# Kernel optimization log

Hardware: AMD Instinct MI355X
Metric: run time of the kernel (lower is better)

## Reference

```python
import jax, jax.numpy as jnp
import numpy as np

EPS = 1e-5
BN_SCALE = 1.0 / np.sqrt(1.0 + EPS)  # inference BN with running_mean=0, running_var=1


def lrelu(x):
    return jnp.where(x >= 0, x, 0.2 * x)


def bn_affine(x, g, b, axis=1):
    shp = [1] * x.ndim
    shp[axis] = -1
    return x * (g.reshape(shp) * BN_SCALE) + b.reshape(shp)


def knn_idx(x, k):
    # x: (B, C, N) -> (B, N, k) indices of k nearest neighbors (incl. self)
    x2 = jnp.sum(x * x, axis=1)                       # (B, N)
    inner = jnp.einsum('bcn,bcm->bnm', x, x)          # (B, N, N)
    neg_dist = 2.0 * inner - x2[:, :, None] - x2[:, None, :]
    return jax.lax.top_k(neg_dist, k)[1]


def graph_feature(x, k):
    # x: (B, C, N) -> (B, 2C, N, k) edge features [x_j - x_i, x_i]
    B, C, N = x.shape
    idx = knn_idx(x, k)                               # (B, N, k)
    xt = jnp.transpose(x, (0, 2, 1))                  # (B, N, C)
    nbr = xt[jnp.arange(B)[:, None, None], idx]       # (B, N, k, C)
    ctr = xt[:, :, None, :]                           # (B, N, 1, C)
    feat = jnp.concatenate([nbr - ctr, jnp.broadcast_to(ctr, nbr.shape)], axis=-1)
    return jnp.transpose(feat, (0, 3, 1, 2))          # (B, 2C, N, k)


def edge_conv(x, W, g, b, k):
    # get_graph_feature -> 1x1 conv -> BN -> LeakyReLU -> max over neighbors
    f = graph_feature(x, k)
    h = jnp.einsum('oc,bcnk->bonk', W, f)
    return jnp.max(lrelu(bn_affine(h, g, b, axis=1)), axis=-1)  # (B, O, N)


def fps(xyz, m):
    # xyz: (B, 3, N) -> (B, m) farthest-point-sample indices, starting at index 0
    B, _, N = xyz.shape
    pts = jnp.transpose(xyz, (0, 2, 1))               # (B, N, 3)

    def body(carry, _):
        dists, last = carry
        p = jnp.take_along_axis(pts, last[:, None, None], axis=1)  # (B, 1, 3)
        d = jnp.sum((pts - p) ** 2, axis=-1)          # (B, N)
        dists = jnp.minimum(dists, d)
        nxt = jnp.argmax(dists, axis=-1).astype(jnp.int32)
        return (dists, nxt), last

    init = (jnp.full((B, N), 1e10, dtype=xyz.dtype), jnp.zeros((B,), jnp.int32))
    _, idxs = jax.lax.scan(body, init, None, length=m)
    return jnp.transpose(idxs, (1, 0))                # (B, m)


def gather_ch(x, idx):
    # x: (B, C, N), idx: (B, M) -> (B, C, M)
    B, C, _ = x.shape
    return jnp.take_along_axis(x, jnp.broadcast_to(idx[:, None, :], (B, C, idx.shape[1])), axis=2)


def aggregate(xyz, node, features, k):
    # xyz: (B,3,N), node: (B,3,M), features: (B,C,N) -> (B,C,M)
    B = xyz.shape[0]
    x2 = jnp.sum(xyz * xyz, axis=1)                   # (B, N)
    n2 = jnp.sum(node * node, axis=1)                 # (B, M)
    inner = jnp.einsum('bcm,bcn->bmn', node, xyz)     # (B, M, N)
    neg_d = 2.0 * inner - n2[:, :, None] - x2[:, None, :]
    idx = jax.lax.top_k(neg_d, k)[1]                  # (B, M, k) nearest points per node
    ft = jnp.transpose(features, (0, 2, 1))           # (B, N, C)
    grp = ft[jnp.arange(B)[:, None, None], idx]       # (B, M, k, C)
    return jnp.transpose(jnp.max(grp, axis=2), (0, 2, 1))  # (B, C, M)


def setup_inputs() -> dict:
    key = jax.random.key(0)
    ks = jax.random.split(key, 32)
    B, N, K, E = 8, 2048, 20, 1024

    def w(k_, o, c):
        return jax.random.normal(k_, (o, c), jnp.float32) / np.sqrt(c)

    def gb(k_, c):
        k1, k2 = jax.random.split(k_)
        return (jax.random.uniform(k1, (c,), jnp.float32, 0.5, 1.5),
                0.1 * jax.random.normal(k2, (c,), jnp.float32))

    g1, b1 = gb(ks[1], 64); g2, b2 = gb(ks[2], 64); g2m, b2m = gb(ks[3], E)
    g3, b3 = gb(ks[4], 256); g4, b4 = gb(ks[5], 256); g5, b5 = gb(ks[6], E)
    g6, b6 = gb(ks[7], 512); g7, b7 = gb(ks[8], 256)
    return {
        'x': jax.random.normal(ks[0], (B, 3, N), jnp.float32),
        'W1': w(ks[10], 64, 6), 'g1': g1, 'b1': b1,
        'W2': w(ks[11], 64, 128), 'g2': g2, 'b2': b2,
        'W2m': w(ks[12], E, 128), 'g2m': g2m, 'b2m': b2m,
        'W3': w(ks[13], 256, 512), 'g3': g3, 'b3': b3,
        'W4': w(ks[14], 256, 512), 'g4': g4, 'b4': b4,
        'W5': w(ks[15], E, 512), 'g5': g5, 'b5': b5,
        'Wl1': w(ks[16], 512, 2 * E), 'g6': g6, 'b6': b6,
        'Wl2': w(ks[17], 256, 512), 'bl2': 0.01 * jax.random.normal(ks[18], (256,), jnp.float32),
        'g7': g7, 'b7': b7,
        'Wl3': w(ks[19], 40, 256), 'bl3': 0.01 * jax.random.normal(ks[20], (40,), jnp.float32),
    }


def reference(x, W1, g1, b1, W2, g2, b2, W2m, g2m, b2m, W3, g3, b3,
              W4, g4, b4, W5, g5, b5, Wl1, g6, b6, Wl2, bl2, g7, b7, Wl3, bl3):
    K = 20
    B, _, N = x.shape
    xyz = x

    x1 = edge_conv(x, W1, g1, b1, K)                  # (B, 64, N)
    x2 = edge_conv(x1, W2, g2, b2, K)                 # (B, 64, N)
    xt1_ = jnp.concatenate([x1, x2], axis=1)          # (B, 128, N)
    xt1 = lrelu(bn_affine(jnp.einsum('oc,bcn->bon', W2m, xt1_), g2m, b2m, axis=1))

    idx = fps(xyz, N // 4)                            # (B, N/4)
    node1 = gather_ch(xyz, idx)                       # (B, 3, N/4)
    nf1 = gather_ch(xt1_, idx)                        # (B, 128, N/4)
    agg = aggregate(xyz, node1, xt1_, K)              # (B, 128, N/4)
    xm = jnp.concatenate([nf1, agg], axis=1)          # (B, 256, N/4)

    x3 = edge_conv(xm, W3, g3, b3, K // 2)            # (B, 256, N/4)
    x4 = edge_conv(x3, W4, g4, b4, K // 2)            # (B, 256, N/4)
    xt2 = lrelu(bn_affine(jnp.einsum('oc,bcn->bon', W5, jnp.concatenate([x3, x4], axis=1)), g5, b5, axis=1))

    v = jnp.concatenate([jnp.max(xt1, axis=-1), jnp.max(xt2, axis=-1)], axis=1)  # (B, 2E)
    h = lrelu(bn_affine(v @ Wl1.T, g6, b6, axis=1))   # dropout = identity (eval)
    h = lrelu(bn_affine(h @ Wl2.T + bl2, g7, b7, axis=1))
    logits = h @ Wl3.T + bl3                          # (B, 40)
    return (logits, node1)
```

## Files before the change

kernel.cpp:

```cpp
#include <hip/hip_runtime.h>

#define BN_SCALE 0.9999950000374997f

template <int CTRL>
__device__ __forceinline__ float dpp_fmax_step(float v) {
  int xi = __builtin_bit_cast(int, v);
  int ti = __builtin_amdgcn_update_dpp(xi, xi, CTRL, 0xf, 0xf, false);
  return fmaxf(v, __builtin_bit_cast(float, ti));
}
template <int CTRL>
__device__ __forceinline__ int dpp_imin_step(int v) {
  int t = __builtin_amdgcn_update_dpp(v, v, CTRL, 0xf, 0xf, false);
  return (t < v) ? t : v;
}
template <int CTRL>
__device__ __forceinline__ float dpp_fadd_step(float v) {
  int ti = __builtin_amdgcn_update_dpp(0, __builtin_bit_cast(int, v), CTRL, 0xf, 0xf, true);
  return v + __builtin_bit_cast(float, ti);
}
__device__ __forceinline__ float wave_fmax(float v) {
  v = dpp_fmax_step<0x111>(v);
  v = dpp_fmax_step<0x112>(v);
  v = dpp_fmax_step<0x114>(v);
  v = dpp_fmax_step<0x118>(v);
  v = dpp_fmax_step<0x142>(v);
  v = dpp_fmax_step<0x143>(v);
  return __builtin_bit_cast(float, __builtin_amdgcn_readlane(__builtin_bit_cast(int, v), 63));
}
__device__ __forceinline__ int wave_imin(int v) {
  v = dpp_imin_step<0x111>(v);
  v = dpp_imin_step<0x112>(v);
  v = dpp_imin_step<0x114>(v);
  v = dpp_imin_step<0x118>(v);
  v = dpp_imin_step<0x142>(v);
  v = dpp_imin_step<0x143>(v);
  return __builtin_amdgcn_readlane(v, 63);
}
__device__ __forceinline__ float wave_fadd(float v) {
  v = dpp_fadd_step<0x111>(v);
  v = dpp_fadd_step<0x112>(v);
  v = dpp_fadd_step<0x114>(v);
  v = dpp_fadd_step<0x118>(v);
  v = dpp_fadd_step<0x142>(v);
  v = dpp_fadd_step<0x143>(v);
  return __builtin_bit_cast(float, __builtin_amdgcn_readlane(__builtin_bit_cast(int, v), 63));
}

template <int R, bool SQPRE>
__device__ __forceinline__ void knn4_body(const float* __restrict__ Q, int qStrideB,
                                          const float* __restrict__ Xc, int cStrideB,
                                          int C, int M, int N, int k, int* __restrict__ idxOut,
                                          const float* __restrict__ sqPre,
                                          int b, int q0, char* smem) {
  constexpr int NR = 4 * R;
  float (*negd)[R * 256] = (float (*)[R * 256])smem;
  int tid = threadIdx.x;
  const float* qb = Q + (long)b * qStrideB + q0;
  const float* cb = Xc + (long)b * cStrideB;
  if constexpr (R % 4 == 0) {
    constexpr int H = R / 4;
    float d0[R], d1[R], d2[R], d3[R], sq[R];
    #pragma unroll
    for (int i = 0; i < R; ++i) { d0[i] = d1[i] = d2[i] = d3[i] = sq[i] = 0.f; }
    for (int c = 0; c < C; ++c) {
      float4 q4 = *(const float4*)(qb + (long)c * M);
      const float4* pc4 = (const float4*)(cb + (long)c * N);
      #pragma unroll
      for (int h = 0; h < H; ++h) {
        float4 xv = pc4[tid + 256 * h];
        if (!SQPRE) {
          sq[4 * h + 0] = fmaf(xv.x, xv.x, sq[4 * h + 0]);
          sq[4 * h + 1] = fmaf(xv.y, xv.y, sq[4 * h + 1]);
          sq[4 * h + 2] = fmaf(xv.z, xv.z, sq[4 * h + 2]);
          sq[4 * h + 3] = fmaf(xv.w, xv.w, sq[4 * h + 3]);
        }
        d0[4 * h + 0] = fmaf(q4.x, xv.x, d0[4 * h + 0]);
        d0[4 * h + 1] = fmaf(q4.x, xv.y, d0[4 * h + 1]);
        d0[4 * h + 2] = fmaf(q4.x, xv.z, d0[4 * h + 2]);
        d0[4 * h + 3] = fmaf(q4.x, xv.w, d0[4 * h + 3]);
        d1[4 * h + 0] = fmaf(q4.y, xv.x, d1[4 * h + 0]);
        d1[4 * h + 1] = fmaf(q4.y, xv.y, d1[4 * h + 1]);
        d1[4 * h + 2] = fmaf(q4.y, xv.z, d1[4 * h + 2]);
        d1[4 * h + 3] = fmaf(q4.y, xv.w, d1[4 * h + 3]);
        d2[4 * h + 0] = fmaf(q4.z, xv.x, d2[4 * h + 0]);
        d2[4 * h + 1] = fmaf(q4.z, xv.y, d2[4 * h + 1]);
        d2[4 * h + 2] = fmaf(q4.z, xv.z, d2[4 * h + 2]);
        d2[4 * h + 3] = fmaf(q4.z, xv.w, d2[4 * h + 3]);
        d3[4 * h + 0] = fmaf(q4.w, xv.x, d3[4 * h + 0]);
        d3[4 * h + 1] = fmaf(q4.w, xv.y, d3[4 * h + 1]);
        d3[4 * h + 2] = fmaf(q4.w, xv.z, d3[4 * h + 2]);
        d3[4 * h + 3] = fmaf(q4.w, xv.w, d3[4 * h + 3]);
      }
    }
    #pragma unroll
    for (int h = 0; h < H; ++h) {
      float4 s4;
      if (SQPRE) {
        s4 = ((const float4*)(sqPre + (long)b * N))[tid + 256 * h];
      } else {
        s4 = make_float4(sq[4 * h], sq[4 * h + 1], sq[4 * h + 2], sq[4 * h + 3]);
      }
      ((float4*)negd[0])[tid + 256 * h] =
          make_float4(2.f * d0[4 * h] - s4.x, 2.f * d0[4 * h + 1] - s4.y,
                      2.f * d0[4 * h + 2] - s4.z, 2.f * d0[4 * h + 3] - s4.w);
      ((float4*)negd[1])[tid + 256 * h] =
          make_float4(2.f * d1[4 * h] - s4.x, 2.f * d1[4 * h + 1] - s4.y,
                      2.f * d1[4 * h + 2] - s4.z, 2.f * d1[4 * h + 3] - s4.w);
      ((float4*)negd[2])[tid + 256 * h] =
          make_float4(2.f * d2[4 * h] - s4.x, 2.f * d2[4 * h + 1] - s4.y,
                      2.f * d2[4 * h + 2] - s4.z, 2.f * d2[4 * h + 3] - s4.w);
      ((float4*)negd[3])[tid + 256 * h] =
          make_float4(2.f * d3[4 * h] - s4.x, 2.f * d3[4 * h + 1] - s4.y,
                      2.f * d3[4 * h + 2] - s4.z, 2.f * d3[4 * h + 3] - s4.w);
    }
  } else {
    float d0[R], d1[R], d2[R], d3[R], sq[R];
    #pragma unroll
    for (int i = 0; i < R; ++i) { d0[i] = d1[i] = d2[i] = d3[i] = sq[i] = 0.f; }
    for (int c = 0; c < C; ++c) {
      float4 q4 = *(const float4*)(qb + (long)c * M);
      const float* pc = cb + (long)c * N;
      #pragma unroll
      for (int i = 0; i < R; ++i) {
        float xv = pc[tid + 256 * i];
        sq[i] = fmaf(xv, xv, sq[i]);
        d0[i] = fmaf(q4.x, xv, d0[i]);
        d1[i] = fmaf(q4.y, xv, d1[i]);
        d2[i] = fmaf(q4.z, xv, d2[i]);
        d3[i] = fmaf(q4.w, xv, d3[i]);
      }
    }
    #pragma unroll
    for (int i = 0; i < R; ++i) {
      int m = tid + 256 * i;
      negd[0][m] = 2.f * d0[i] - sq[i];
      negd[1][m] = 2.f * d1[i] - sq[i];
      negd[2][m] = 2.f * d2[i] - sq[i];
      negd[3][m] = 2.f * d3[i] - sq[i];
    }
  }
  __syncthreads();
  int lane = tid & 63, w = tid >> 6;
  const float* row = negd[w];
  int* outp = idxOut + ((long)b * M + (q0 + w)) * k;
  float v[NR];
  #pragma unroll
  for (int i = 0; i < NR; ++i) v[i] = row[lane + 64 * i];
  constexpr int G = NR / 4;
  float bv[G]; int br[G];
  #pragma unroll
  for (int g = 0; g < G; ++g) {
    float v0 = v[4 * g]; int r0 = 4 * g;
    #pragma unroll
    for (int j = 1; j < 4; ++j) {
      bool c = v[4 * g + j] > v0;
      v0 = c ? v[4 * g + j] : v0;
      r0 = c ? (4 * g + j) : r0;
    }
    bv[g] = v0; br[g] = r0;
  }
  for (int kk = 0; kk < k; ++kk) {
    float mv[G]; int mi[G];
    #pragma unroll
    for (int g = 0; g < G; ++g) { mv[g] = bv[g]; mi[g] = br[g]; }
    #pragma unroll
    for (int s = G >> 1; s >= 1; s >>= 1) {
      #pragma unroll
      for (int i = 0; i < s; ++i) {
        bool c = mv[2 * i] >= mv[2 * i + 1];
        mv[i] = c ? mv[2 * i] : mv[2 * i + 1];
        mi[i] = c ? mi[2 * i] : mi[2 * i + 1];
      }
    }
    float best = mv[0]; int ib = mi[0];
    int bi = (best > -INFINITY) ? (lane + (ib << 6)) : N;
    float gmax = wave_fmax(best);
    int cand = (best == gmax) ? bi : 0x7FFFFFFF;
    int big = wave_imin(cand);
    if (lane == 0) outp[kk] = big;
    int ri = big >> 6;
    bool mine = (lane == (big & 63));
    #pragma unroll
    for (int i = 0; i < NR; ++i)
      if (i == ri) v[i] = mine ? -INFINITY : v[i];
    int gi = ri >> 2;
    #pragma unroll
    for (int g = 0; g < G; ++g) {
      if (g == gi) {
        float v0 = v[4 * g]; int r0 = 4 * g;
        #pragma unroll
        for (int j = 1; j < 4; ++j) {
          bool c = v[4 * g + j] > v0;
          v0 = c ? v[4 * g + j] : v0;
          r0 = c ? (4 * g + j) : r0;
        }
        bv[g] = v0; br[g] = r0;
      }
    }
  }
}

template <int R>
__global__ void knn4_kernel(const float* __restrict__ Q, int qStrideB,
                            const float* __restrict__ Xc, int cStrideB,
                            int C, int M, int N, int k, int* __restrict__ idxOut) {
  __shared__ __align__(16) char smem[R * 256 * 4 * 4];
  knn4_body<R, false>(Q, qStrideB, Xc, cStrideB, C, M, N, k, idxOut, nullptr,
                      blockIdx.y, blockIdx.x * 4, smem);
}

__device__ __forceinline__ void gemmPS_body(const float* __restrict__ X, int xStrideB, int C, int Np,
                                            const float* __restrict__ W, int ldw, int O,
                                            float* __restrict__ PtT, float* __restrict__ StT,
                                            int b, int n0, int o0, char* smem) {
  float (*Wp)[68] = (float (*)[68])smem;
  float (*Ws)[68] = (float (*)[68])(smem + 4352);
  float (*Xt)[68] = (float (*)[68])(smem + 8704);
  int tid = threadIdx.x;
  int to = tid % 16, tn = tid / 16;
  float accP[4][4] = {}, accS[4][4] = {};
  for (int c0 = 0; c0 < C; c0 += 16) {
    for (int e = tid; e < 16 * 64; e += 256) {
      int oo = e / 16, kk = e % 16;
      int c = c0 + kk, o = o0 + oo;
      bool ok = (c < C && o < O);
      Wp[kk][oo] = ok ? W[(long)o * ldw + c] : 0.f;
      Ws[kk][oo] = ok ? W[(long)o * ldw + C + c] : 0.f;
    }
    for (int e = tid; e < 16 * 64; e += 256) {
      int kk = e / 64, nn = e % 64;
      int c = c0 + kk, n = n0 + nn;
      Xt[kk][nn] = (c < C && n < Np) ? X[(long)b * xStrideB + (long)c * Np + n] : 0.f;
    }
    __syncthreads();
    for (int kk = 0; kk < 16; ++kk) {
      float4 xv = *(const float4*)&Xt[kk][tn * 4];
      float4 wp = *(const float4*)&Wp[kk][to * 4];
      float4 ws = *(const float4*)&Ws[kk][to * 4];
      float xs[4] = {xv.x, xv.y, xv.z, xv.w};
      float wps[4] = {wp.x, wp.y, wp.z, wp.w};
      float wss[4] = {ws.x, ws.y, ws.z, ws.w};
      #pragma unroll
      for (int i = 0; i < 4; ++i)
        #pragma unroll
        for (int j = 0; j < 4; ++j) {
          accP[i][j] = fmaf(xs[i], wps[j], accP[i][j]);
          accS[i][j] = fmaf(xs[i], wss[j], accS[i][j]);
        }
    }
    __syncthreads();
  }
  #pragma unroll
  for (int i = 0; i < 4; ++i) {
    int n = n0 + tn * 4 + i;
    if (n >= Np) continue;
    int o = o0 + to * 4;
    if (o + 3 < O) {
      long off = ((long)b * Np + n) * O + o;
      *(float4*)&PtT[off] = make_float4(accP[i][0], accP[i][1], accP[i][2], accP[i][3]);
      *(float4*)&StT[off] = make_float4(accS[i][0], accS[i][1], accS[i][2], accS[i][3]);
    } else {
      for (int j = 0; j < 4; ++j) {
        int oo = o + j;
        if (oo < O) {
          long off = ((long)b * Np + n) * O + oo;
          PtT[off] = accP[i][j];
          StT[off] = accS[i][j];
        }
      }
    }
  }
}

__device__ __forceinline__ void ecfinish_body64(const float* __restrict__ Pt, const float* __restrict__ St,
                                                const int* __restrict__ idx, int k, int O, int Np,
                                                const float* __restrict__ g, const float* __restrict__ bb,
                                                float* __restrict__ outp, long oStrideB,
                                                float* __restrict__ sqOut,
                                                int b, int blk) {
  int tid = threadIdx.x;
  int o = tid & 63;
  int n = blk * 4 + (tid >> 6);
  const float* PtB = Pt + (long)b * Np * O;
  const float* StB = St + (long)b * Np * O;
  const int* ip = idx + ((long)b * Np + n) * k;
  float mx = -INFINITY, mn = INFINITY;
  for (int kk = 0; kk < k; ++kk) {
    float v = PtB[(long)ip[kk] * O + o];
    mx = fmaxf(mx, v); mn = fminf(mn, v);
  }
  float ctrP = PtB[(long)n * O + o];
  float ctrS = StB[(long)n * O + o];
  float gs = g[o] * BN_SCALE;
  float m = (gs >= 0.f) ? mx : mn;
  float h = (ctrS - ctrP + m) * gs + bb[o];
  float out = h >= 0.f ? h : 0.2f * h;
  outp[(long)b * oStrideB + (long)o * Np + n] = out;
  if (sqOut) {
    int obits = __builtin_bit_cast(int, out);
    float acc = 0.f;
    #pragma unroll
    for (int c = 0; c < 64; ++c) {
      float hv = __builtin_bit_cast(float, __builtin_amdgcn_readlane(obits, c));
      acc = fmaf(hv, hv, acc);
    }
    if (o == 0) sqOut[(long)b * Np + n] = acc;
  }
}

__global__ void ecfinish_kernel(const float* __restrict__ Pt, const float* __restrict__ St,
                                const int* __restrict__ idx, int k, int O, int Np,
                                const float* __restrict__ g, const float* __restrict__ bb,
                                float* __restrict__ outp, long oStrideB) {
  int b = blockIdx.y;
  int n = blockIdx.x * blockDim.y + threadIdx.y;
  int o = threadIdx.x;
  const float* PtB = Pt + (long)b * Np * O;
  const float* StB = St + (long)b * Np * O;
  const int* ip = idx + ((long)b * Np + n) * k;
  float mx = -INFINITY, mn = INFINITY;
  for (int kk = 0; kk < k; ++kk) {
    float v = PtB[(long)ip[kk] * O + o];
    mx = fmaxf(mx, v); mn = fminf(mn, v);
  }
  float ctrP = PtB[(long)n * O + o];
  float ctrS = StB[(long)n * O + o];
  float gs = g[o] * BN_SCALE;
  float m = (gs >= 0.f) ? mx : mn;
  float h = (ctrS - ctrP + m) * gs + bb[o];
  outp[(long)b * oStrideB + (long)o * Np + n] = h >= 0.f ? h : 0.2f * h;
}

__device__ __forceinline__ void gemm_colmax_body(const float* __restrict__ X, int xStrideB, int C, int Np,
                                                 const float* __restrict__ W, int ldw, int O,
                                                 const float* __restrict__ g, const float* __restrict__ bb,
                                                 float* __restrict__ partial,
                                                 int b, int n0, int o0, int nt, int nNT, char* smem) {
  float (*Wt)[68] = (float (*)[68])smem;
  float (*Xt)[68] = (float (*)[68])(smem + 4352);
  int tid = threadIdx.x;
  int to = tid % 16, tn = tid / 16;
  float acc[4][4] = {};
  for (int c0 = 0; c0 < C; c0 += 16) {
    for (int e = tid; e < 16 * 64; e += 256) {
      int oo = e / 16, kk = e % 16;
      int c = c0 + kk, o = o0 + oo;
      Wt[kk][oo] = (c < C && o < O) ? W[(long)o * ldw + c] : 0.f;
    }
    for (int e = tid; e < 16 * 64; e += 256) {
      int kk = e / 64, nn = e % 64;
      int c = c0 + kk, n = n0 + nn;
      Xt[kk][nn] = (c < C && n < Np) ? X[(long)b * xStrideB + (long)c * Np + n] : 0.f;
    }
    __syncthreads();
    for (int kk = 0; kk < 16; ++kk) {
      float4 xv = *(const float4*)&Xt[kk][tn * 4];
      float4 wv = *(const float4*)&Wt[kk][to * 4];
      float xs[4] = {xv.x, xv.y, xv.z, xv.w};
      float wvs[4] = {wv.x, wv.y, wv.z, wv.w};
      #pragma unroll
      for (int i = 0; i < 4; ++i)
        #pragma unroll
        for (int j = 0; j < 4; ++j) acc[i][j] = fmaf(xs[i], wvs[j], acc[i][j]);
    }
    __syncthreads();
  }
  float vm[4];
  #pragma unroll
  for (int j = 0; j < 4; ++j) {
    int o = o0 + to * 4 + j;
    float gs = g[o] * BN_SCALE, bo = bb[o];
    float m = -INFINITY;
    #pragma unroll
    for (int i = 0; i < 4; ++i) {
      float h = acc[i][j] * gs + bo;
      h = h >= 0.f ? h : 0.2f * h;
      m = fmaxf(m, h);
    }
    vm[j] = m;
  }
  #pragma unroll
  for (int j = 0; j < 4; ++j) Xt[tn][to * 4 + j] = vm[j];
  __syncthreads();
  for (int s = 8; s > 0; s >>= 1) {
    if (tn < s)
      for (int j = 0; j < 4; ++j)
        Xt[tn][to * 4 + j] = fmaxf(Xt[tn][to * 4 + j], Xt[tn + s][to * 4 + j]);
    __syncthreads();
  }
  if (tn == 0)
    for (int j = 0; j < 4; ++j) {
      int o = o0 + to * 4 + j;
      partial[((long)b * nNT + nt) * O + o] = Xt[0][to * 4 + j];
    }
}

__global__ void gemm_colmax_kernel(const float* __restrict__ X, int xStrideB, int C, int Np,
                                   const float* __restrict__ W, int ldw, int O,
                                   const float* __restrict__ g, const float* __restrict__ bb,
                                   float* __restrict__ partial) {
  __shared__ __align__(16) char smem[8704];
  gemm_colmax_body(X, xStrideB, C, Np, W, ldw, O, g, bb, partial,
                   blockIdx.z, blockIdx.x * 64, blockIdx.y * 64, blockIdx.x, gridDim.x, smem);
}

__device__ __forceinline__ void xmfill_body(const float* __restrict__ xt1, int N,
                                            const int* __restrict__ fpsI,
                                            const int* __restrict__ idxA, int k, int M,
                                            float* __restrict__ xm, int xe) {
  long t = (long)xe * 256 + threadIdx.x;
  int i = (int)(t % M);
  int c = (int)((t / M) % 128);
  int b = (int)(t / ((long)128 * M));
  const float* xb = xt1 + (long)b * 128 * N + (long)c * N;
  float* xmB = xm + (long)b * 256 * M;
  xmB[(long)c * M + i] = xb[fpsI[(long)b * M + i]];
  const int* ip = idxA + ((long)b * M + i) * k;
  float best = -INFINITY;
  for (int kk = 0; kk < k; ++kk) best = fmaxf(best, xb[ip[kk]]);
  xmB[(long)(128 + c) * M + i] = best;
}

template <int FIRST, int LAST>
__device__ __forceinline__ void fps_body_rg(const float* __restrict__ xyz, int N, int M,
                                            int it0, int it1,
                                            int* __restrict__ fpsIdx, float* __restrict__ node1,
                                            float* __restrict__ distSv, int* __restrict__ lastSv,
                                            int b, char* smem) {
  #pragma clang fp contract(off)
  float* px = (float*)smem;
  float* py = (float*)(smem + 8192);
  float* pz = (float*)(smem + 16384);
  int*   fidx = (int*)(smem + 24576);
  float4* wvc = (float4*)(smem + 26624);
  int*   wis  = (int*)(smem + 26752);
  int tid = threadIdx.x;
  int lane = tid & 63, w = tid >> 6;
  const float* xb = xyz + (long)b * 3 * N;
  for (int n = tid; n < N; n += 256) {
    int s = ((n & 7) << 8) | (n >> 3);
    px[s] = xb[n]; py[s] = xb[N + n]; pz[s] = xb[2 * N + n];
  }
  if (!FIRST) {
    for (int e = tid; e < it0; e += 256) fidx[e] = fpsIdx[(long)b * M + e];
  }
  __syncthreads();
  float ptx[8], pty[8], ptz[8];
  #pragma unroll
  for (int i = 0; i < 8; ++i) {
    int s = (i << 8) | tid;
    ptx[i] = px[s]; pty[i] = py[s]; ptz[i] = pz[s];
  }
  float dist[8];
  int last;
  float lx, ly, lz;
  if (FIRST) {
    #pragma unroll
    for (int i = 0; i < 8; ++i) dist[i] = 1e10f;
    last = 0;
    int s0 = 0;
    lx = px[s0]; ly = py[s0]; lz = pz[s0];
  } else {
    #pragma unroll
    for (int i = 0; i < 8; ++i) dist[i] = distSv[(long)b * 2048 + i * 256 + tid];
    last = lastSv[b];
    int sl = ((last & 7) << 8) | (last >> 3);
    lx = px[sl]; ly = py[sl]; lz = pz[sl];
  }
  int base = tid * 8;
  for (int it = it0; it < it1; ++it) {
    int p = it & 1;
    if (tid == 0) fidx[it] = last;
    float best = -INFINITY; int bi = N;
    #pragma unroll
    for (int i = 0; i < 8; ++i) {
      float dx = ptx[i] - lx, dy = pty[i] - ly, dz = ptz[i] - lz;
      float dx2 = dx * dx, dy2 = dy * dy, dz2 = dz * dz;
      float d = (dx2 + dy2) + dz2;
      float dn = dist[i];
      if (d < dn) dn = d;
      dist[i] = dn;
      if (dn > best) { best = dn; bi = base + i; }
    }
    float cx = ptx[0], cy = pty[0], cz = ptz[0];
    #pragma unroll
    for (int i = 1; i < 8; ++i) {
      bool c = (bi == base + i);
      cx = c ? ptx[i] : cx; cy = c ? pty[i] : cy; cz = c ? ptz[i] : cz;
    }
    float gmax = wave_fmax(best);
    unsigned long long mm = __ballot(best == gmax);
    int srcLane = (int)(__ffsll((long long)mm) - 1);
    if (lane == srcLane) { wvc[p * 4 + w] = make_float4(gmax, cx, cy, cz); wis[p * 4 + w] = bi; }
    __syncthreads();
    float4 c0 = wvc[p * 4 + 0], c1 = wvc[p * 4 + 1], c2 = wvc[p * 4 + 2], c3 = wvc[p * 4 + 3];
    int i0 = wis[p * 4 + 0], i1 = wis[p * 4 + 1], i2 = wis[p * 4 + 2], i3 = wis[p * 4 + 3];
    float bv = c0.x; int bbi = i0; lx = c0.y; ly = c0.z; lz = c0.w;
    { bool c = (c1.x > bv) || (c1.x == bv && i1 < bbi);
      bv = c ? c1.x : bv; bbi = c ? i1 : bbi; lx = c ? c1.y : lx; ly = c ? c1.z : ly; lz = c ? c1.w : lz; }
    { bool c = (c2.x > bv) || (c2.x == bv && i2 < bbi);
      bv = c ? c2.x : bv; bbi = c ? i2 : bbi; lx = c ? c2.y : lx; ly = c ? c2.z : ly; lz = c ? c2.w : lz; }
    { bool c = (c3.x > bv) || (c3.x == bv && i3 < bbi);
      bv = c ? c3.x : bv; bbi = c ? i3 : bbi; lx = c ? c3.y : lx; ly = c ? c3.z : ly; lz = c ? c3.w : lz; }
    last = bbi;
  }
  if (!LAST) {
    for (int e = tid; e < it1; e += 256) {
      if (e >= it0) fpsIdx[(long)b * M + e] = fidx[e];
    }
    #pragma unroll
    for (int i = 0; i < 8; ++i) distSv[(long)b * 2048 + i * 256 + tid] = dist[i];
    if (tid == 0) lastSv[b] = last;
  } else {
    for (int e = tid; e < M; e += 256) fpsIdx[(long)b * M + e] = fidx[e];
    for (int e = tid; e < 3 * M; e += 256) {
      int c = e / M, i = e % M;
      int src = fidx[i];
      int s = ((src & 7) << 8) | (src >> 3);
      node1[(long)b * 3 * M + e] = (c == 0) ? px[s] : (c == 1) ? py[s] : pz[s];
    }
  }
}

template <int FIRST, int LAST, bool SQP>
__global__ void knnfpsgemm_kernel(const float* __restrict__ Q, int qStrideB,
                                  const float* __restrict__ Xc, int cStrideB,
                                  int C, int Mq, int N, int k, int* __restrict__ idxOut,
                                  const float* __restrict__ W, int ldw, int O,
                                  float* __restrict__ Pt, float* __restrict__ St,
                                  const float* __restrict__ xyz, int Mf, int it0, int it1,
                                  int* __restrict__ fpsIdx, float* __restrict__ node1,
                                  float* __restrict__ distSv, int* __restrict__ lastSv,
                                  const float* __restrict__ sqPre,
                                  int nQblk, int nGblk, int nB) {
  __shared__ __align__(16) char smem[32768];
  int bid = blockIdx.x;
  if (bid < nB) {
    __builtin_amdgcn_s_setprio(3);
    fps_body_rg<FIRST, LAST>(xyz, N, Mf, it0, it1, fpsIdx, node1, distSv, lastSv, bid, smem);
    __builtin_amdgcn_s_setprio(0);
  } else if (bid < nB + nB * nQblk) {
    int e = bid - nB;
    knn4_body<8, SQP>(Q, qStrideB, Xc, cStrideB, C, Mq, N, k, idxOut, sqPre,
                      e / nQblk, (e % nQblk) * 4, smem);
  } else {
    int e = bid - nB - nB * nQblk;
    gemmPS_body(Xc, cStrideB, C, N, W, ldw, O, Pt, St,
                e / nGblk, (e % nGblk) * 64, 0, smem);
  }
}

__global__ void ecfps_kernel(const float* __restrict__ Pt, const float* __restrict__ St,
                             const int* __restrict__ idx, int k, int O, int Np,
                             const float* __restrict__ g, const float* __restrict__ bb,
                             float* __restrict__ outp, long oStrideB,
                             float* __restrict__ sqOut,
                             const float* __restrict__ xyz, int N, int Mf, int it0, int it1,
                             int* __restrict__ fpsIdx, float* __restrict__ node1,
                             float* __restrict__ distSv, int* __restrict__ lastSv,
                             int nEperB, int nB) {
  __shared__ __align__(16) char smem[26784];
  int bid = blockIdx.x;
  if (bid < nB) {
    __builtin_amdgcn_s_setprio(3);
    fps_body_rg<0, 0>(xyz, N, Mf, it0, it1, fpsIdx, node1, distSv, lastSv, bid, smem);
    __builtin_amdgcn_s_setprio(0);
  } else {
    int e = bid - nB;
    ecfinish_body64(Pt, St, idx, k, O, Np, g, bb, outp, oStrideB, sqOut,
                    e / nEperB, e % nEperB);
  }
}

__global__ void ecfagg_kernel(const float* __restrict__ Pt, const float* __restrict__ St,
                              const int* __restrict__ idxS2, int k2, int O2, int Np2,
                              const float* __restrict__ g2, const float* __restrict__ b2,
                              float* __restrict__ out2, long oStrideB2,
                              const float* __restrict__ Qn, int qStrideB,
                              const float* __restrict__ Xc, int cStrideB,
                              int Cq, int Mq, int Nc, int kq, int* __restrict__ idxAgg,
                              int nQblk, int nEperB) {
  __shared__ __align__(16) char smem[32768];
  int bid = blockIdx.x;
  if (bid % 5 == 0) {
    int a = bid / 5;
    knn4_body<8, false>(Qn, qStrideB, Xc, cStrideB, Cq, Mq, Nc, kq, idxAgg, nullptr,
                        a / nQblk, (a % nQblk) * 4, smem);
  } else {
    int e = bid - bid / 5 - 1;
    ecfinish_body64(Pt, St, idxS2, k2, O2, Np2, g2, b2, out2, oStrideB2, nullptr,
                    e / nEperB, e % nEperB);
  }
}

__global__ void colmaxxm_kernel(const float* __restrict__ X, int xStrideB, int C, int Np,
                                const float* __restrict__ W, int ldw, int O,
                                const float* __restrict__ g, const float* __restrict__ bb,
                                float* __restrict__ partial, int nNT, int nOT,
                                const float* __restrict__ xt1, int N,
                                const int* __restrict__ fpsI, const int* __restrict__ idxA,
                                int kq, int M, float* __restrict__ xm) {
  __shared__ __align__(16) char smem[8704];
  int bid = blockIdx.x;
  if (bid % 3 == 0) {
    xmfill_body(xt1, N, fpsI, idxA, kq, M, xm, bid / 3);
  } else {
    int e = bid - bid / 3 - 1;
    int per = nNT * nOT;
    int b = e / per, r = e % per;
    int nt = r % nNT, ot = r / nNT;
    gemm_colmax_body(X, xStrideB, C, Np, W, ldw, O, g, bb, partial,
                     b, nt * 64, ot * 64, nt, nNT, smem);
  }
}

__global__ void knngemm_kernel(const float* __restrict__ Xin, int xStrideB,
                               int C, int Mq, int N, int k, int* __restrict__ idxOut,
                               const float* __restrict__ W, int ldw, int O,
                               float* __restrict__ Pt, float* __restrict__ St,
                               int nQblk, int nGn, int nGo, int nB) {
  __shared__ __align__(16) char smem[13056];
  int bid = blockIdx.x;
  if (bid < nB * nQblk) {
    knn4_body<2, false>(Xin, xStrideB, Xin, xStrideB, C, Mq, N, k, idxOut, nullptr,
                        bid / nQblk, (bid % nQblk) * 4, smem);
  } else {
    int e = bid - nB * nQblk;
    int per = nGn * nGo;
    int b = e / per, r = e % per;
    int nt = r % nGn, ot = r / nGn;
    gemmPS_body(Xin, xStrideB, C, N, W, ldw, O, Pt, St, b, nt * 64, ot * 64, smem);
  }
}

__global__ void headv_kernel(const float* __restrict__ partA, int NTa,
                             const float* __restrict__ partB, int NTb,
                             float* __restrict__ vws) {
  int b = blockIdx.x, tid = threadIdx.x;
  for (int o = tid; o < 1024; o += 256) {
    float m = -INFINITY;
    for (int t = 0; t < NTa; ++t) m = fmaxf(m, partA[((long)b * NTa + t) * 1024 + o]);
    vws[(long)b * 2048 + o] = m;
    float m2 = -INFINITY;
    for (int t = 0; t < NTb; ++t) m2 = fmaxf(m2, partB[((long)b * NTb + t) * 1024 + o]);
    vws[(long)b * 2048 + 1024 + o] = m2;
  }
}

__global__ void headl1_kernel(const float* __restrict__ vws,
                              const float* __restrict__ Wl1, const float* __restrict__ g6,
                              const float* __restrict__ b6, float* __restrict__ h1ws) {
  int tid = threadIdx.x;
  int lane = tid & 63, w = tid >> 6;
  int o0 = blockIdx.x * 8;
  for (int oo = w; oo < 8; oo += 4) {
    int o = o0 + oo;
    const float4* wr = (const float4*)(Wl1 + (long)o * 2048);
    float4 w4[8];
    #pragma unroll
    for (int j = 0; j < 8; ++j) w4[j] = wr[lane + 64 * j];
    float gs = g6[o] * BN_SCALE, bo = b6[o];
    for (int b = 0; b < 8; ++b) {
      const float4* vp = (const float4*)(vws + (long)b * 2048);
      float s = 0.f;
      #pragma unroll
      for (int j = 0; j < 8; ++j) {
        float4 v4 = vp[lane + 64 * j];
        s = fmaf(w4[j].x, v4.x, s); s = fmaf(w4[j].y, v4.y, s);
        s = fmaf(w4[j].z, v4.z, s); s = fmaf(w4[j].w, v4.w, s);
      }
      float t = wave_fadd(s);
      if (lane == 0) {
        float h = t * gs + bo;
        h1ws[(long)b * 512 + o] = h >= 0.f ? h : 0.2f * h;
      }
    }
  }
}

__global__ void headl2_kernel(const float* __restrict__ h1ws,
                              const float* __restrict__ Wl2, const float* __restrict__ bl2,
                              const float* __restrict__ g7, const float* __restrict__ b7,
                              float* __restrict__ h2ws) {
  int tid = threadIdx.x;
  int lane = tid & 63, w = tid >> 6;
  int o0 = blockIdx.x * 8;
  for (int oo = w; oo < 8; oo += 4) {
    int o = o0 + oo;
    const float4* wr = (const float4*)(Wl2 + (long)o * 512);
    float4 w4[2];
    #pragma unroll
    for (int j = 0; j < 2; ++j) w4[j] = wr[lane + 64 * j];
    float bl = bl2[o], gs = g7[o] * BN_SCALE, bo = b7[o];
    for (int b = 0; b < 8; ++b) {
      const float4* hp = (const float4*)(h1ws + (long)b * 512);
      float s = 0.f;
      #pragma unroll
      for (int j = 0; j < 2; ++j) {
        float4 v4 = hp[lane + 64 * j];
        s = fmaf(w4[j].x, v4.x, s); s = fmaf(w4[j].y, v4.y, s);
        s = fmaf(w4[j].z, v4.z, s); s = fmaf(w4[j].w, v4.w, s);
      }
      float t = wave_fadd(s);
      if (lane == 0) {
        float sb = t + bl;
        float h = sb * gs + bo;
        h2ws[(long)b * 256 + o] = h >= 0.f ? h : 0.2f * h;
      }
    }
  }
}

__global__ void headl3_kernel(const float* __restrict__ h2ws,
                              const float* __restrict__ Wl3, const float* __restrict__ bl3,
                              float* __restrict__ logits) {
  int b = blockIdx.x, tid = threadIdx.x;
  int lane = tid & 63, w = tid >> 6;
  const float4* hp = (const float4*)(h2ws + (long)b * 256);
  float4 v4 = hp[lane];
  for (int o = w; o < 40; o += 4) {
    const float4* wr = (const float4*)(Wl3 + (long)o * 256);
    float4 w4 = wr[lane];
    float s = fmaf(w4.x, v4.x, 0.f);
    s = fmaf(w4.y, v4.y, s); s = fmaf(w4.z, v4.z, s); s = fmaf(w4.w, v4.w, s);
    float t = wave_fadd(s);
    if (lane == 0) logits[(long)b * 40 + o] = t + bl3[o];
  }
}

extern "C" void kernel_launch(void* const* d_in, const int* in_sizes, int n_in,
                              void* d_out, int out_size, void* d_ws, size_t ws_size,
                              hipStream_t stream) {
  const float* x   = (const float*)d_in[0];
  const float* W1  = (const float*)d_in[1];
  const float* g1  = (const float*)d_in[2];
  const float* b1  = (const float*)d_in[3];
  const float* W2  = (const float*)d_in[4];
  const float* g2  = (const float*)d_in[5];
  const float* b2  = (const float*)d_in[6];
  const float* W2m = (const float*)d_in[7];
  const float* g2m = (const float*)d_in[8];
  const float* b2m = (const float*)d_in[9];
  const float* W3  = (const float*)d_in[10];
  const float* g3  = (const float*)d_in[11];
  const float* b3  = (const float*)d_in[12];
  const float* W4  = (const float*)d_in[13];
  const float* g4  = (const float*)d_in[14];
  const float* b4  = (const float*)d_in[15];
  const float* W5  = (const float*)d_in[16];
  const float* g5  = (const float*)d_in[17];
  const float* b5  = (const float*)d_in[18];
  const float* Wl1 = (const float*)d_in[19];
  const float* g6  = (const float*)d_in[20];
  const float* b6  = (const float*)d_in[21];
  const float* Wl2 = (const float*)d_in[22];
  const float* bl2 = (const float*)d_in[23];
  const float* g7  = (const float*)d_in[24];
  const float* b7  = (const float*)d_in[25];
  const float* Wl3 = (const float*)d_in[26];
  const float* bl3 = (const float*)d_in[27];
  float* outF = (float*)d_out;

  const int B = 8, N = 2048, K = 20, M = 512, K2 = 10;

  float* ws    = (float*)d_ws;
  float* xt1   = ws;
  float* xm    = xt1 + (size_t)B * 128 * N;
  float* xc    = xm  + (size_t)B * 256 * M;
  float* Pt    = xc  + (size_t)B * 512 * M;
  float* St    = Pt  + (size_t)B * N * 64;
  float* partA = St  + (size_t)B * N * 64;
  float* partB = partA + (size_t)B * 32 * 1024;
  int*   idxK  = (int*)(partB + (size_t)B * 8 * 1024);
  int*   fpsI  = idxK + (size_t)B * N * K;
  float* fpsDist = (float*)(fpsI + (size_t)B * M);
  int*   fpsLast = (int*)(fpsDist + (size_t)B * 2048);
  int*   idxAgg  = fpsLast + 64;
  float* sqS2    = (float*)(idxAgg + (size_t)B * M * K);
  float* vws     = sqS2 + (size_t)B * N;
  float* h1ws    = vws + (size_t)B * 2048;
  float* h2ws    = h1ws + (size_t)B * 512;

  float* logits = outF;
  float* node1  = outF + 320;

  dim3 t256(256);
  const int nQblk = N / 4;
  const int nGblk = N / 64;
  const int nFused = B + B * nQblk + B * nGblk;
  const int nQa = M / 4;
  const int IT1 = 208, IT2 = 304;

  knnfpsgemm_kernel<1, 0, false><<<dim3(nFused), t256, 0, stream>>>(
      x, 3 * N, x, 3 * N, 3, N, N, K, idxK,
      W1, 6, 64, Pt, St,
      x, M, 0, IT1, fpsI, node1, fpsDist, fpsLast, nullptr, nQblk, nGblk, B);

  ecfps_kernel<<<dim3(B + B * (N / 4)), t256, 0, stream>>>(
      Pt, St, idxK, K, 64, N, g1, b1, xt1, (long)128 * N, sqS2,
      x, N, M, IT1, IT2, fpsI, node1, fpsDist, fpsLast, N / 4, B);

  knnfpsgemm_kernel<0, 1, true><<<dim3(nFused), t256, 0, stream>>>(
      xt1, 128 * N, xt1, 128 * N, 64, N, N, K, idxK,
      W2, 128, 64, Pt, St,
      x, M, IT2, M, fpsI, node1, fpsDist, fpsLast, sqS2, nQblk, nGblk, B);

  ecfagg_kernel<<<dim3(B * nQa + B * (N / 4)), t256, 0, stream>>>(
      Pt, St, idxK, K, 64, N, g2, b2, xt1 + (size_t)64 * N, (long)128 * N,
      node1, 3 * M, x, 3 * N, 3, M, N, K, idxAgg, nQa, N / 4);

  colmaxxm_kernel<<<dim3((B * 128 * M) / 256 + B * 32 * 16), t256, 0, stream>>>(
      xt1, 128 * N, 128, N, W2m, 128, 1024, g2m, b2m, partA, 32, 16,
      xt1, N, fpsI, idxAgg, K, M, xm);

  knngemm_kernel<<<dim3(B * nQa + B * (M / 64) * (256 / 64)), t256, 0, stream>>>(
      xm, 256 * M, 256, M, M, K2, idxK, W3, 512, 256, Pt, St, nQa, M / 64, 256 / 64, B);
  ecfinish_kernel<<<dim3(M, B), dim3(256, 1), 0, stream>>>(Pt, St, idxK, K2, 256, M, g3, b3, xc, (long)512 * M);

  knngemm_kernel<<<dim3(B * nQa + B * (M / 64) * (256 / 64)), t256, 0, stream>>>(
      xc, 512 * M, 256, M, M, K2, idxK, W4, 512, 256, Pt, St, nQa, M / 64, 256 / 64, B);
  ecfinish_kernel<<<dim3(M, B), dim3(256, 1), 0, stream>>>(Pt, St, idxK, K2, 256, M, g4, b4,
                                                           xc + (size_t)256 * M, (long)512 * M);

  gemm_colmax_kernel<<<dim3(M / 64, 1024 / 64, B), t256, 0, stream>>>(xc, 512 * M, 512, M, W5, 512, 1024,
                                                                      g5, b5, partB);

  headv_kernel<<<dim3(B), t256, 0, stream>>>(partA, N / 64, partB, M / 64, vws);
  headl1_kernel<<<dim3(64), t256, 0, stream>>>(vws, Wl1, g6, b6, h1ws);
  headl2_kernel<<<dim3(32), t256, 0, stream>>>(h1ws, Wl2, bl2, g7, b7, h2ws);
  headl3_kernel<<<dim3(B), t256, 0, stream>>>(h2ws, Wl3, bl3, logits);
}
```

Before: 970.2 us.

## Run farthest-point sampling on a single wavefront without block barriers

The FPS loop now runs on one 64-lane wavefront per batch instead of four wavefronts. Each lane tracks 32 distances and reads point coordinates from LDS every iteration, so the per-iteration __syncthreads and the cross-wave LDS reduction are gone. The argmax tie-break becomes a wave-level integer min over candidate indices. In exchange, each lane does four times the arithmetic per iteration and re-reads coordinates from LDS, and the three idle wavefronts leave the block early.

```diff
diff --git a/kernel.cpp b/kernel.cpp
--- a/kernel.cpp
+++ b/kernel.cpp
@@ -432,92 +432,67 @@
   float* py = (float*)(smem + 8192);
   float* pz = (float*)(smem + 16384);
   int*   fidx = (int*)(smem + 24576);
-  float4* wvc = (float4*)(smem + 26624);
-  int*   wis  = (int*)(smem + 26752);
   int tid = threadIdx.x;
-  int lane = tid & 63, w = tid >> 6;
   const float* xb = xyz + (long)b * 3 * N;
   for (int n = tid; n < N; n += 256) {
-    int s = ((n & 7) << 8) | (n >> 3);
-    px[s] = xb[n]; py[s] = xb[N + n]; pz[s] = xb[2 * N + n];
+    px[n] = xb[n]; py[n] = xb[N + n]; pz[n] = xb[2 * N + n];
   }
   if (!FIRST) {
     for (int e = tid; e < it0; e += 256) fidx[e] = fpsIdx[(long)b * M + e];
   }
   __syncthreads();
-  float ptx[8], pty[8], ptz[8];
-  #pragma unroll
-  for (int i = 0; i < 8; ++i) {
-    int s = (i << 8) | tid;
-    ptx[i] = px[s]; pty[i] = py[s]; ptz[i] = pz[s];
-  }
-  float dist[8];
+  if (tid >= 64) return;
+  int lane = tid;
+  float dist[32];
   int last;
   float lx, ly, lz;
   if (FIRST) {
     #pragma unroll
-    for (int i = 0; i < 8; ++i) dist[i] = 1e10f;
+    for (int i = 0; i < 32; ++i) dist[i] = 1e10f;
     last = 0;
-    int s0 = 0;
-    lx = px[s0]; ly = py[s0]; lz = pz[s0];
+    lx = px[0]; ly = py[0]; lz = pz[0];
   } else {
     #pragma unroll
-    for (int i = 0; i < 8; ++i) dist[i] = distSv[(long)b * 2048 + i * 256 + tid];
+    for (int i = 0; i < 32; ++i) dist[i] = distSv[(long)b * 2048 + i * 64 + lane];
     last = lastSv[b];
-    int sl = ((last & 7) << 8) | (last >> 3);
-    lx = px[sl]; ly = py[sl]; lz = pz[sl];
-  }
-  int base = tid * 8;
+    lx = px[last]; ly = py[last]; lz = pz[last];
+  }
   for (int it = it0; it < it1; ++it) {
-    int p = it & 1;
-    if (tid == 0) fidx[it] = last;
-    float best = -INFINITY; int bi = N;
-    #pragma unroll
-    for (int i = 0; i < 8; ++i) {
-      float dx = ptx[i] - lx, dy = pty[i] - ly, dz = ptz[i] - lz;
+    if (lane == 0) fidx[it] = last;
+    float best = -INFINITY; int ib = 0;
+    #pragma unroll
+    for (int i = 0; i < 32; ++i) {
+      float X = px[i * 64 + lane], Y = py[i * 64 + lane], Z = pz[i * 64 + lane];
+      float dx = X - lx, dy = Y - ly, dz = Z - lz;
       float dx2 = dx * dx, dy2 = dy * dy, dz2 = dz * dz;
       float d = (dx2 + dy2) + dz2;
       float dn = dist[i];
       if (d < dn) dn = d;
       dist[i] = dn;
-      if (dn > best) { best = dn; bi = base + i; }
-    }
-    float cx = ptx[0], cy = pty[0], cz = ptz[0];
-    #pragma unroll
-    for (int i = 1; i < 8; ++i) {
-      bool c = (bi == base + i);
-      cx = c ? ptx[i] : cx; cy = c ? pty[i] : cy; cz = c ? ptz[i] : cz;
-    }
+      bool c = dn > best;
+      best = c ? dn : best;
+      ib = c ? i : ib;
+    }
+    int bi = (ib << 6) + lane;
     float gmax = wave_fmax(best);
-    unsigned long long mm = __ballot(best == gmax);
-    int srcLane = (int)(__ffsll((long long)mm) - 1);
-    if (lane == srcLane) { wvc[p * 4 + w] = make_float4(gmax, cx, cy, cz); wis[p * 4 + w] = bi; }
-    __syncthreads();
-    float4 c0 = wvc[p * 4 + 0], c1 = wvc[p * 4 + 1], c2 = wvc[p * 4 + 2], c3 = wvc[p * 4 + 3];
-    int i0 = wis[p * 4 + 0], i1 = wis[p * 4 + 1], i2 = wis[p * 4 + 2], i3 = wis[p * 4 + 3];
-    float bv = c0.x; int bbi = i0; lx = c0.y; ly = c0.z; lz = c0.w;
-    { bool c = (c1.x > bv) || (c1.x == bv && i1 < bbi);
-      bv = c ? c1.x : bv; bbi = c ? i1 : bbi; lx = c ? c1.y : lx; ly = c ? c1.z : ly; lz = c ? c1.w : lz; }
-    { bool c = (c2.x > bv) || (c2.x == bv && i2 < bbi);
-      bv = c ? c2.x : bv; bbi = c ? i2 : bbi; lx = c ? c2.y : lx; ly = c ? c2.z : ly; lz = c ? c2.w : lz; }
-    { bool c = (c3.x > bv) || (c3.x == bv && i3 < bbi);
-      bv = c ? c3.x : bv; bbi = c ? i3 : bbi; lx = c ? c3.y : lx; ly = c ? c3.z : ly; lz = c ? c3.w : lz; }
-    last = bbi;
+    int cand = (best == gmax) ? bi : 0x7FFFFFFF;
+    int big = wave_imin(cand);
+    last = big;
+    lx = px[big]; ly = py[big]; lz = pz[big];
   }
   if (!LAST) {
-    for (int e = tid; e < it1; e += 256) {
+    for (int e = lane; e < it1; e += 64) {
       if (e >= it0) fpsIdx[(long)b * M + e] = fidx[e];
     }
     #pragma unroll
-    for (int i = 0; i < 8; ++i) distSv[(long)b * 2048 + i * 256 + tid] = dist[i];
-    if (tid == 0) lastSv[b] = last;
+    for (int i = 0; i < 32; ++i) distSv[(long)b * 2048 + i * 64 + lane] = dist[i];
+    if (lane == 0) lastSv[b] = last;
   } else {
-    for (int e = tid; e < M; e += 256) fpsIdx[(long)b * M + e] = fidx[e];
-    for (int e = tid; e < 3 * M; e += 256) {
+    for (int e = lane; e < M; e += 64) fpsIdx[(long)b * M + e] = fidx[e];
+    for (int e = lane; e < 3 * M; e += 64) {
       int c = e / M, i = e % M;
       int src = fidx[i];
-      int s = ((src & 7) << 8) | (src >> 3);
-      node1[(long)b * 3 * M + e] = (c == 0) ? px[s] : (c == 1) ? py[s] : pz[s];
+      node1[(long)b * 3 * M + e] = (c == 0) ? px[src] : (c == 1) ? py[src] : pz[src];
     }
   }
 }
@@ -559,7 +534,7 @@
                              int* __restrict__ fpsIdx, float* __restrict__ node1,
                              float* __restrict__ distSv, int* __restrict__ lastSv,
                              int nEperB, int nB) {
-  __shared__ __align__(16) char smem[26784];
+  __shared__ __align__(16) char smem[26624];
   int bid = blockIdx.x;
   if (bid < nB) {
     __builtin_amdgcn_s_setprio(3);
```

Result: slower. 1.367 ms (+40.9%).
